# Performance work log

Measured on AMD Instinct MI355X. Metric: run time of the kernel, lower is better.

## Reference

```python
import jax, jax.numpy as jnp
import numpy as np

WIDTH = 2048
NUM_HEADS = 16
HEAD_DIM = WIDTH // NUM_HEADS
WINDOW = 1024
B, T = 4, 2048
MIN_LOGIT = -2.3819763e+38
MAX_WAVELENGTH = 10000.0


def apply_rope(x, positions):
    # x: [b, t, n, h]; RoPE on first half of h, pass-through second half
    b, t, n, h = x.shape
    x_rope, x_pass = jnp.split(x, 2, axis=-1)
    half = x_rope.shape[-1] // 2
    freq_exponents = 2.0 * jnp.arange(half, dtype=jnp.float32) / (2 * half)
    inv_freq = MAX_WAVELENGTH ** (-freq_exponents)  # [half]
    sinusoid = positions.astype(jnp.float32).reshape(1, t, 1, 1) * inv_freq  # [1,t,1,half]
    sin = jnp.sin(sinusoid).astype(x.dtype)
    cos = jnp.cos(sinusoid).astype(x.dtype)
    x1, x2 = jnp.split(x_rope, 2, axis=-1)
    return jnp.concatenate([x1 * cos - x2 * sin, x2 * cos + x1 * sin, x_pass], axis=-1)


def setup_inputs() -> dict:
    key = jax.random.key(0)
    ks = jax.random.split(key, 6)
    x = jax.random.normal(ks[0], (B, T, WIDTH), dtype=jnp.float32)
    segment_pos = jnp.arange(T, dtype=jnp.int32)
    # forward-pass mask: single segment, causal + window
    pos = jnp.arange(T)
    attention_mask = (pos[:, None] >= pos[None, :]) & (pos[:, None] <= pos[None, :] + WINDOW)
    std = np.sqrt(1.0 / WIDTH)
    wq = jax.random.normal(ks[1], (WIDTH, WIDTH), dtype=jnp.float32) * std
    wk = jax.random.normal(ks[2], (HEAD_DIM, WIDTH), dtype=jnp.float32) * std
    wv = jax.random.normal(ks[3], (HEAD_DIM, WIDTH), dtype=jnp.float32) * std
    w_out = jax.random.normal(ks[4], (WIDTH, WIDTH), dtype=jnp.float32) * std
    b_out = jnp.zeros((WIDTH,), dtype=jnp.float32)
    return {"x": x, "segment_pos": segment_pos, "attention_mask": attention_mask,
            "wq": wq, "wk": wk, "wv": wv, "w_out": w_out, "b_out": b_out}


def reference(x, segment_pos, attention_mask, wq, wk, wv, w_out, b_out):
    b, t, _ = x.shape
    q = (x @ wq.T).reshape(b, t, NUM_HEADS, HEAD_DIM)  # [b,t,n,h]
    k = (x @ wk.T).reshape(b, t, 1, HEAD_DIM)          # single shared KV head (MQA)
    v = x @ wv.T                                        # [b,t,h]
    q = apply_rope(q, segment_pos)
    k = apply_rope(k, segment_pos)[:, :, 0]             # [b,t,h]
    logits = jnp.einsum('btnh,bsh->bnts', q, k).astype(jnp.float32) * (HEAD_DIM ** -0.5)
    logits = jnp.where(attention_mask[None, None], logits, MIN_LOGIT)
    probs = jax.nn.softmax(logits, axis=-1).astype(x.dtype)
    encoded = jnp.einsum('bnts,bsh->btnh', probs, v).reshape(b, t, WIDTH)
    return encoded @ w_out.T + b_out
```

## Files before the change

### kernel.cpp

```cpp
#include <hip/hip_runtime.h>
#include <stdint.h>


#define WIDTH_ 2048
#define NHEADS_ 16
#define HD_ 128
#define WINDOW_ 1024
#define B_ 4
#define T_ 2048
#define MROWS_ (B_ * T_)
#define NQKV_ (WIDTH_ + 2 * HD_)

typedef float f32x4 __attribute__((ext_vector_type(4)));
typedef __bf16 bf16x8 __attribute__((ext_vector_type(8)));
typedef float f32x4v __attribute__((ext_vector_type(4)));
typedef unsigned short u16;
typedef unsigned int u32;

__device__ __forceinline__ u16 f2bf(float x) {
  u32 u = __builtin_bit_cast(u32, x);
  return (u16)((u + 0x7FFFu + ((u >> 16) & 1u)) >> 16);
}
__device__ __forceinline__ float bf2f(u16 b) {
  u32 u = ((u32)b) << 16;
  return __builtin_bit_cast(float, u);
}
__device__ __forceinline__ u32 pack2bf(float a, float b) {
  union { __bf16 h[2]; u32 u; } c;
  c.h[0] = (__bf16)a; c.h[1] = (__bf16)b;
  return c.u;
}

__device__ __forceinline__ f32x4 mfma16(bf16x8 a, bf16x8 b, f32x4 c) {
  return __builtin_amdgcn_mfma_f32_16x16x32_bf16(a, b, c, 0, 0, 0);
}

#define GLL16(gp, lp)                                          \
  __builtin_amdgcn_global_load_lds(                            \
      (const __attribute__((address_space(1))) void*)(gp),     \
      (__attribute__((address_space(3))) void*)(lp), 16, 0, 0)

#define CSC_ 0.12753101296631838f

__global__ __launch_bounds__(256) void cvt_f32_bf16(const float* __restrict__ src,
                                                    u16* __restrict__ dst, int n4) {
  int i = blockIdx.x * blockDim.x + threadIdx.x;
  int stride = gridDim.x * blockDim.x;
  for (; i < n4; i += stride) {
    f32x4v v = *reinterpret_cast<const f32x4v*>(src + 4 * (size_t)i);
    u32 lo = (u32)f2bf(v[0]) | ((u32)f2bf(v[1]) << 16);
    u32 hi = (u32)f2bf(v[2]) | ((u32)f2bf(v[3]) << 16);
    uint2 o;
    o.x = lo; o.y = hi;
    *reinterpret_cast<uint2*>(dst + 4 * (size_t)i) = o;
  }
}

__global__ __launch_bounds__(256) void cvt_weights(const float* __restrict__ wq,
                                                   const float* __restrict__ wk,
                                                   const float* __restrict__ wv,
                                                   const float* __restrict__ wo,
                                                   u16* __restrict__ wqkv,
                                                   u16* __restrict__ wob) {
  const int NQ = WIDTH_ * WIDTH_ / 4;
  const int NK = HD_ * WIDTH_ / 4;
  const int total = 2 * NQ + 2 * NK;
  int i = blockIdx.x * blockDim.x + threadIdx.x;
  int stride = gridDim.x * blockDim.x;
  for (; i < total; i += stride) {
    const float* s;
    u16* d;
    int j;
    if (i < NQ) { s = wq; d = wqkv; j = i; }
    else if (i < NQ + NK) { s = wk; d = wqkv + (size_t)WIDTH_ * WIDTH_; j = i - NQ; }
    else if (i < NQ + 2 * NK) { s = wv; d = wqkv + (size_t)(WIDTH_ + HD_) * WIDTH_; j = i - NQ - NK; }
    else { s = wo; d = wob; j = i - NQ - 2 * NK; }
    f32x4v v = *reinterpret_cast<const f32x4v*>(s + 4 * (size_t)j);
    uint2 o;
    o.x = (u32)f2bf(v[0]) | ((u32)f2bf(v[1]) << 16);
    o.y = (u32)f2bf(v[2]) | ((u32)f2bf(v[3]) << 16);
    *reinterpret_cast<uint2*>(d + 4 * (size_t)j) = o;
  }
}

template <bool F32OUT>
__global__ __launch_bounds__(256) void gemm_bt(const u16* __restrict__ A,
                                               const u16* __restrict__ W,
                                               void* __restrict__ Cout,
                                               const float* __restrict__ bias,
                                               int M, int N, int K) {
  __shared__ alignas(16) u16 As[128 * 32];
  __shared__ alignas(16) u16 Bs[128 * 32];
  const int tid = threadIdx.x;
  const int wid = tid >> 6, lane = tid & 63;
  const int g = lane >> 4, lr = lane & 15;
  const int m0 = blockIdx.y << 7, n0 = blockIdx.x << 7;
  const int wm = wid >> 1, wn = wid & 1;

  const f32x4 vzero = {0.f, 0.f, 0.f, 0.f};
  f32x4 acc[4][4];
#pragma unroll
  for (int i = 0; i < 4; i++)
#pragma unroll
    for (int j = 0; j < 4; j++) acc[i][j] = vzero;

  const int c0 = wid * 2, c1 = wid * 2 + 1;
  const int lrow = lane >> 2;
  const int lcol = (lane & 3) * 8;
  const u16* a0 = A + (size_t)(m0 + c0 * 16 + lrow) * K + lcol;
  const u16* a1 = A + (size_t)(m0 + c1 * 16 + lrow) * K + lcol;
  const u16* b0 = W + (size_t)(n0 + c0 * 16 + lrow) * K + lcol;
  const u16* b1 = W + (size_t)(n0 + c1 * 16 + lrow) * K + lcol;

  for (int k0 = 0; k0 < K; k0 += 32) {
    __syncthreads();
    GLL16(a0 + k0, &As[c0 * 512]);
    GLL16(a1 + k0, &As[c1 * 512]);
    GLL16(b0 + k0, &Bs[c0 * 512]);
    GLL16(b1 + k0, &Bs[c1 * 512]);
    __syncthreads();

    bf16x8 af[4], bfv[4];
#pragma unroll
    for (int mi = 0; mi < 4; mi++)
      af[mi] = *(const bf16x8*)&As[(wm * 64 + mi * 16 + lr) * 32 + g * 8];
#pragma unroll
    for (int ni = 0; ni < 4; ni++)
      bfv[ni] = *(const bf16x8*)&Bs[(wn * 64 + ni * 16 + lr) * 32 + g * 8];
#pragma unroll
    for (int mi = 0; mi < 4; mi++)
#pragma unroll
      for (int ni = 0; ni < 4; ni++)
        acc[mi][ni] = mfma16(af[mi], bfv[ni], acc[mi][ni]);
  }

#pragma unroll
  for (int mi = 0; mi < 4; mi++) {
    int row = m0 + wm * 64 + mi * 16 + g * 4;
#pragma unroll
    for (int ni = 0; ni < 4; ni++) {
      int col = n0 + wn * 64 + ni * 16 + lr;
#pragma unroll
      for (int r = 0; r < 4; r++) {
        float v = acc[mi][ni][r];
        if (F32OUT) {
          ((float*)Cout)[(size_t)(row + r) * N + col] = v + bias[col];
        } else {
          ((u16*)Cout)[(size_t)(row + r) * N + col] = f2bf(v);
        }
      }
    }
  }
}

template <bool F32OUT>
__global__ __launch_bounds__(512, 2) void gemm256(const u16* __restrict__ A,
                                                  const u16* __restrict__ W,
                                                  void* __restrict__ Cout,
                                                  const float* __restrict__ bias,
                                                  int M, int N, int K) {
  __shared__ alignas(16) u16 As[3][256 * 32];
  __shared__ alignas(16) u16 Bs[3][256 * 32];
  const int tid = threadIdx.x;
  const int wid = tid >> 6, lane = tid & 63;
  const int g = lane >> 4, lr = lane & 15;
  const int wm = wid >> 2, wn = wid & 3;

  const int nwg = gridDim.x;
  const int o = blockIdx.x;
  const int wg = (o & 7) * (nwg >> 3) + (o >> 3);
  const int NT = N >> 8;
  const int mt = wg / NT, nt = wg % NT;
  const int m0 = mt << 8, n0 = nt << 8;

  const u16* pa[2];
  const u16* pb[2];
#pragma unroll
  for (int j = 0; j < 2; j++) {
    int row = wid * 32 + j * 16 + (lane >> 2);
    int sc = (lane & 3) ^ ((row >> 1) & 3);
    pa[j] = A + (size_t)(m0 + row) * K + sc * 8;
    pb[j] = W + (size_t)(n0 + row) * K + sc * 8;
  }
  const int ldsoff = wid * 2048;

  const f32x4 vzero = {0.f, 0.f, 0.f, 0.f};
  f32x4 acc[8][4];
#pragma unroll
  for (int i = 0; i < 8; i++)
#pragma unroll
    for (int j = 0; j < 4; j++) acc[i][j] = vzero;

#define STAGE_A(bi, k0)                                        \
  do {                                                         \
    GLL16(pa[0] + (k0), (char*)As[bi] + ldsoff);               \
    GLL16(pa[1] + (k0), (char*)As[bi] + ldsoff + 1024);        \
  } while (0)
#define STAGE_B(bi, k0)                                        \
  do {                                                         \
    GLL16(pb[0] + (k0), (char*)Bs[bi] + ldsoff);               \
    GLL16(pb[1] + (k0), (char*)Bs[bi] + ldsoff + 1024);        \
  } while (0)

  STAGE_A(0, 0); STAGE_B(0, 0);
  STAGE_A(1, 32); STAGE_B(1, 32);
  asm volatile("s_waitcnt vmcnt(4)" ::: "memory");
  __builtin_amdgcn_sched_barrier(0);
  __builtin_amdgcn_s_barrier();

  const int ntk = K >> 5;
  int cur = 0;
  for (int t = 0; t < ntk; ++t) {
    const int nx2 = (cur + 2 >= 3) ? cur - 1 : cur + 2;
    const char* aB = (const char*)As[cur];
    const char* bB = (const char*)Bs[cur];
    const bool pre = (t + 2 < ntk);

    bf16x8 bfv[4], af[4];
#pragma unroll
    for (int ni = 0; ni < 4; ni++) {
      int row = wn * 64 + ni * 16 + lr;
      bfv[ni] = *(const bf16x8*)(bB + row * 64 + ((g ^ ((row >> 1) & 3)) << 4));
    }
#pragma unroll
    for (int mi = 0; mi < 4; mi++) {
      int row = wm * 128 + mi * 16 + lr;
      af[mi] = *(const bf16x8*)(aB + row * 64 + ((g ^ ((row >> 1) & 3)) << 4));
    }
    if (pre) STAGE_A(nx2, (t + 2) << 5);
    __builtin_amdgcn_s_barrier();
    asm volatile("s_waitcnt lgkmcnt(0)" ::: "memory");
    __builtin_amdgcn_sched_barrier(0);
    __builtin_amdgcn_s_setprio(1);
#pragma unroll
    for (int mi = 0; mi < 4; mi++)
#pragma unroll
      for (int ni = 0; ni < 4; ni++)
        acc[mi][ni] = mfma16(af[mi], bfv[ni], acc[mi][ni]);
    __builtin_amdgcn_s_setprio(0);
    __builtin_amdgcn_s_barrier();

    bf16x8 af2[4];
#pragma unroll
    for (int mi = 0; mi < 4; mi++) {
      int row = wm * 128 + 64 + mi * 16 + lr;
      af2[mi] = *(const bf16x8*)(aB + row * 64 + ((g ^ ((row >> 1) & 3)) << 4));
    }
    if (pre) STAGE_B(nx2, (t + 2) << 5);
    __builtin_amdgcn_s_barrier();
    asm volatile("s_waitcnt lgkmcnt(0)" ::: "memory");
    __builtin_amdgcn_sched_barrier(0);
    __builtin_amdgcn_s_setprio(1);
#pragma unroll
    for (int mi = 0; mi < 4; mi++)
#pragma unroll
      for (int ni = 0; ni < 4; ni++)
        acc[mi + 4][ni] = mfma16(af2[mi], bfv[ni], acc[mi + 4][ni]);
    __builtin_amdgcn_s_setprio(0);

    if (pre) {
      asm volatile("s_waitcnt vmcnt(4)" ::: "memory");
    } else if (t + 1 < ntk) {
      asm volatile("s_waitcnt vmcnt(0)" ::: "memory");
    }
    __builtin_amdgcn_sched_barrier(0);
    __builtin_amdgcn_s_barrier();

    cur = (cur + 1 >= 3) ? 0 : cur + 1;
  }
#undef STAGE_A
#undef STAGE_B

#pragma unroll
  for (int mi = 0; mi < 8; mi++) {
    int row = m0 + wm * 128 + mi * 16 + g * 4;
#pragma unroll
    for (int ni = 0; ni < 4; ni++) {
      int col = n0 + wn * 64 + ni * 16 + lr;
#pragma unroll
      for (int r = 0; r < 4; r++) {
        float v = acc[mi][ni][r];
        if (F32OUT) {
          ((float*)Cout)[(size_t)(row + r) * N + col] = v + bias[col];
        } else {
          ((u16*)Cout)[(size_t)(row + r) * N + col] = f2bf(v);
        }
      }
    }
  }
}

__global__ __launch_bounds__(256) void rope_scatter(const u16* __restrict__ Qraw,
                                                    const u16* __restrict__ KVraw,
                                                    const int* __restrict__ segpos,
                                                    u16* __restrict__ Qb,
                                                    u16* __restrict__ Kb,
                                                    u16* __restrict__ VT) {
  const int row = blockIdx.x;
  const int b = row / T_, t = row % T_;
  const float pos = (float)segpos[t];
  const u16* qsrc = Qraw + (size_t)row * WIDTH_;
  const u16* kvsrc = KVraw + (size_t)row * 256;
  const int tid = threadIdx.x;
  const float L2_10K_OVER_32 = 0.4152410118609203f;

  for (int j = tid; j < NHEADS_ * 32; j += 256) {
    int h = j >> 5, d = j & 31;
    float inv = exp2f(-(float)d * L2_10K_OVER_32);
    float ang = pos * inv;
    float sn = sinf(ang), cs = cosf(ang);
    int c1 = h * HD_ + d, c2 = c1 + 32;
    float x1 = bf2f(qsrc[c1]), x2 = bf2f(qsrc[c2]);
    Qb[(size_t)row * WIDTH_ + c1] = f2bf((x1 * cs - x2 * sn) * CSC_);
    Qb[(size_t)row * WIDTH_ + c2] = f2bf((x2 * cs + x1 * sn) * CSC_);
  }
  for (int j = tid; j < NHEADS_ * 64; j += 256) {
    int h = j >> 6, d = j & 63;
    int c = h * HD_ + 64 + d;
    Qb[(size_t)row * WIDTH_ + c] = f2bf(bf2f(qsrc[c]) * CSC_);
  }
  if (tid < 32) {
    int d = tid;
    float inv = exp2f(-(float)d * L2_10K_OVER_32);
    float ang = pos * inv;
    float sn = sinf(ang), cs = cosf(ang);
    float x1 = bf2f(kvsrc[d]), x2 = bf2f(kvsrc[d + 32]);
    Kb[(size_t)row * HD_ + d] = f2bf(x1 * cs - x2 * sn);
    Kb[(size_t)row * HD_ + d + 32] = f2bf(x2 * cs + x1 * sn);
  } else if (tid >= 64 && tid < 128) {
    int d = tid;
    Kb[(size_t)row * HD_ + d] = kvsrc[d];
  }
  for (int j = tid; j < HD_; j += 256) {
    VT[((size_t)b * HD_ + j) * T_ + t] = kvsrc[HD_ + j];
  }
}

__global__ __launch_bounds__(512, 4) void attn(const u16* __restrict__ Qb,
                                               const u16* __restrict__ Kb,
                                               const u16* __restrict__ VT,
                                               u16* __restrict__ Eb) {
  __shared__ alignas(16) u16 Ks[2][64 * 128];
  __shared__ alignas(16) u16 Vs[2][128 * 64];
  __shared__ alignas(16) u16 Ps[8][16 * 64];

  const int tid = threadIdx.x;
  const int wid = tid >> 6, lane = tid & 63;
  const int g = lane >> 4, lr = lane & 15;

  const int bid = blockIdx.x;
  const int grp = bid >> 4;
  const int b = grp >> 4, n = grp & 15;
  const int qt = ((bid & 15) + b * 4) & 15;
  const int q0b = qt * 128;
  const int q0w = q0b + wid * 16;

  const char* kptr = (const char*)(Kb + (size_t)b * T_ * HD_);
  const char* vptr = (const char*)(VT + (size_t)b * HD_ * T_);

  const char* srcb[4];
  int smul, dst0;
  if (wid < 4) {
    smul = HD_ * 2;
#pragma unroll
    for (int i = 0; i < 4; i++) {
      int row = wid * 16 + i * 4 + (lane >> 4);
      int c = (lane & 15) << 4;
      srcb[i] = kptr + (size_t)row * 256 + (c ^ ((row & 7) << 4));
    }
    dst0 = wid * 4096;
  } else {
    smul = 2;
#pragma unroll
    for (int i = 0; i < 4; i++) {
      int row = (wid - 4) * 32 + i * 8 + (lane >> 3);
      int c = (lane & 7) << 4;
      srcb[i] = vptr + (size_t)row * (T_ * 2) + (c ^ ((row & 7) << 4));
    }
    dst0 = (wid - 4) * 4096;
  }

  bf16x8 qf[4];
  {
    const u16* qrow = Qb + (size_t)(b * T_ + q0w + lr) * WIDTH_ + n * HD_;
#pragma unroll
    for (int kk = 0; kk < 4; kk++) qf[kk] = *(const bf16x8*)(qrow + kk * 32 + g * 8);
  }

  const f32x4 vzero = {0.f, 0.f, 0.f, 0.f};
  f32x4 eacc[8];
#pragma unroll
  for (int i = 0; i < 8; i++) eacc[i] = vzero;
  float m_r = -1e30f, l_r = 0.f;

  const int sbeg = (q0b > WINDOW_) ? (q0b - WINDOW_) : 0;
  const int nt = (q0b + 127 - sbeg) / 64 + 1;

  char* Pw = (char*)Ps[wid];
  const int swz = (lr & 7) << 4;
  const int q = q0w + lr;

  auto STAGE = [&](int s0, int buf) {
    char* dbase = (wid < 4) ? ((char*)Ks[buf] + dst0) : ((char*)Vs[buf] + dst0);
#pragma unroll
    for (int i = 0; i < 4; i++) {
      GLL16(srcb[i] + (size_t)s0 * smul, dbase + i * 1024);
    }
  };

  STAGE(sbeg, 0);
  __syncthreads();

  for (int t = 0; t < nt; ++t) {
    const int s0 = sbeg + t * 64;
    const int cur = t & 1;
    if (t + 1 < nt) STAGE(s0 + 64, cur ^ 1);

    const bool active = (s0 <= q0w + 15) && (s0 + 63 >= q0w - WINDOW_);
    if (active) {
      const char* kB = (const char*)Ks[cur];
      const char* vB = (const char*)Vs[cur];
      f32x4 sacc[4];
#pragma unroll
      for (int h = 0; h < 4; h++) sacc[h] = vzero;
#pragma unroll
      for (int h = 0; h < 4; h++) {
        const int krow = h * 16 + lr;
#pragma unroll
        for (int kk = 0; kk < 4; kk++) {
          bf16x8 kf = *(const bf16x8*)(kB + krow * 256 + ((kk * 64 + g * 16) ^ swz));
          sacc[h] = mfma16(kf, qf[kk], sacc[h]);
        }
      }

      const bool wint = (s0 + 63 <= q0w) && (s0 >= q0w + 15 - WINDOW_);
      float pm = -1e30f;
      if (wint) {
#pragma unroll
        for (int h = 0; h < 4; h++)
#pragma unroll
          for (int r = 0; r < 4; r++) pm = fmaxf(pm, sacc[h][r]);
      } else {
#pragma unroll
        for (int h = 0; h < 4; h++)
#pragma unroll
          for (int r = 0; r < 4; r++) {
            int s = s0 + h * 16 + g * 4 + r;
            bool ok = (s <= q) && (s + WINDOW_ >= q);
            float v = ok ? sacc[h][r] : -1e30f;
            sacc[h][r] = v;
            pm = fmaxf(pm, v);
          }
      }
      pm = fmaxf(pm, __shfl_xor(pm, 16));
      pm = fmaxf(pm, __shfl_xor(pm, 32));

      if (!__all(pm <= m_r + 8.f)) {
        float mnew = fmaxf(m_r, pm);
        float alpha = exp2f(m_r - mnew);
        m_r = mnew;
        l_r *= alpha;
        float aq[4];
#pragma unroll
        for (int r = 0; r < 4; r++) aq[r] = __shfl(alpha, g * 4 + r);
#pragma unroll
        for (int i = 0; i < 8; i++) {
          f32x4 e = eacc[i];
#pragma unroll
          for (int r = 0; r < 4; r++) e[r] *= aq[r];
          eacc[i] = e;
        }
      }
      float rs = 0.f;
#pragma unroll
      for (int h = 0; h < 4; h++)
#pragma unroll
        for (int r = 0; r < 4; r++) {
          float e = exp2f(sacc[h][r] - m_r);
          sacc[h][r] = e;
          rs += e;
        }
      rs += __shfl_xor(rs, 16);
      rs += __shfl_xor(rs, 32);
      l_r += rs;

#pragma unroll
      for (int h = 0; h < 4; h++) {
        int base = (lr * 128 + h * 32 + g * 8) ^ swz;
        uint2 w2;
        w2.x = pack2bf(sacc[h][0], sacc[h][1]);
        w2.y = pack2bf(sacc[h][2], sacc[h][3]);
        *(uint2*)(Pw + base) = w2;
      }
      bf16x8 pf0 = *(const bf16x8*)(Pw + ((lr * 128 + g * 16) ^ swz));
      bf16x8 pf1 = *(const bf16x8*)(Pw + ((lr * 128 + 64 + g * 16) ^ swz));

#pragma unroll
      for (int ht = 0; ht < 8; ht++) {
        const int vrow = ht * 16 + lr;
        bf16x8 vf0 = *(const bf16x8*)(vB + vrow * 128 + ((g * 16) ^ swz));
        bf16x8 vf1 = *(const bf16x8*)(vB + vrow * 128 + ((64 + g * 16) ^ swz));
        eacc[ht] = mfma16(pf0, vf0, eacc[ht]);
        eacc[ht] = mfma16(pf1, vf1, eacc[ht]);
      }
    }
    __syncthreads();
  }

  float lq[4];
#pragma unroll
  for (int r = 0; r < 4; r++) lq[r] = 1.f / __shfl(l_r, g * 4 + r);
#pragma unroll
  for (int ht = 0; ht < 8; ht++) {
#pragma unroll
    for (int r = 0; r < 4; r++) {
      int row = b * T_ + q0w + g * 4 + r;
      int col = n * HD_ + ht * 16 + lr;
      Eb[(size_t)row * WIDTH_ + col] = f2bf(eacc[ht][r] * lq[r]);
    }
  }
}

extern "C" void kernel_launch(void* const* d_in, const int* in_sizes, int n_in,
                              void* d_out, int out_size, void* d_ws, size_t ws_size,
                              hipStream_t stream) {
  (void)in_sizes; (void)n_in; (void)out_size; (void)ws_size;
  const float* x = (const float*)d_in[0];
  const int* segpos = (const int*)d_in[1];
  const float* wq = (const float*)d_in[3];
  const float* wk = (const float*)d_in[4];
  const float* wv = (const float*)d_in[5];
  const float* w_out = (const float*)d_in[6];
  const float* b_out = (const float*)d_in[7];

  char* p = (char*)d_ws;
  u16* xb = (u16*)p;    p += (size_t)MROWS_ * WIDTH_ * 2;
  u16* wqkv = (u16*)p;  p += (size_t)NQKV_ * WIDTH_ * 2;
  u16* wob = (u16*)p;   p += (size_t)WIDTH_ * WIDTH_ * 2;
  u16* qraw = (u16*)p;  p += (size_t)MROWS_ * WIDTH_ * 2;
  u16* kvraw = (u16*)p; p += (size_t)MROWS_ * 256 * 2;
  u16* qb = (u16*)p;    p += (size_t)MROWS_ * WIDTH_ * 2;
  u16* kb = (u16*)p;    p += (size_t)MROWS_ * HD_ * 2;
  u16* vt = (u16*)p;    p += (size_t)B_ * HD_ * T_ * 2;
  u16* eb = xb;

  cvt_f32_bf16<<<4096, 256, 0, stream>>>(x, xb, MROWS_ * WIDTH_ / 4);
  cvt_weights<<<2048, 256, 0, stream>>>(wq, wk, wv, w_out, wqkv, wob);

  gemm256<false><<<(MROWS_ / 256) * (WIDTH_ / 256), 512, 0, stream>>>(
      xb, wqkv, qraw, nullptr, MROWS_, WIDTH_, WIDTH_);
  gemm_bt<false><<<dim3(256 / 128, MROWS_ / 128), 256, 0, stream>>>(
      xb, wqkv + (size_t)WIDTH_ * WIDTH_, kvraw, nullptr, MROWS_, 256, WIDTH_);

  rope_scatter<<<MROWS_, 256, 0, stream>>>(qraw, kvraw, segpos, qb, kb, vt);
  attn<<<B_ * NHEADS_ * (T_ / 128), 512, 0, stream>>>(qb, kb, vt, eb);

  gemm256<true><<<(MROWS_ / 256) * (WIDTH_ / 256), 512, 0, stream>>>(
      eb, wob, d_out, b_out, MROWS_, WIDTH_, WIDTH_);
}
```

Baseline: 341.8 us.

## Fuse Q RoPE into attention and rework GEMM to 64-wide K pipeline

Q RoPE and scaling move out of the scatter kernel and into the attention kernel's Q-fragment load, so the separate Qb buffer is no longer written or re-read. The scatter kernel now handles only K and V with 128 threads. Separately, the 256x256 GEMM is restructured to stage 64-wide K slices in half-tiles, using double buffering and an 8-phase schedule in place of the triple-buffered 32-wide slices. The cost is redundant sin/cos evaluation per head in attention and a new, untested GEMM pipeline whose waitcnt accounting is intricate.

```diff
diff --git a/kernel.cpp b/kernel.cpp
--- a/kernel.cpp
+++ b/kernel.cpp
@@ -41,6 +41,7 @@
       (__attribute__((address_space(3))) void*)(lp), 16, 0, 0)
 
 #define CSC_ 0.12753101296631838f
+#define L2C_ 0.4152410118609203f
 
 __global__ __launch_bounds__(256) void cvt_f32_bf16(const float* __restrict__ src,
                                                     u16* __restrict__ dst, int n4) {
@@ -154,13 +155,13 @@
 }
 
 template <bool F32OUT>
-__global__ __launch_bounds__(512, 2) void gemm256(const u16* __restrict__ A,
-                                                  const u16* __restrict__ W,
-                                                  void* __restrict__ Cout,
-                                                  const float* __restrict__ bias,
-                                                  int M, int N, int K) {
-  __shared__ alignas(16) u16 As[3][256 * 32];
-  __shared__ alignas(16) u16 Bs[3][256 * 32];
+__global__ __launch_bounds__(512, 2) void gemm256p8(const u16* __restrict__ A,
+                                                    const u16* __restrict__ W,
+                                                    void* __restrict__ Cout,
+                                                    const float* __restrict__ bias,
+                                                    int M, int N, int K) {
+  __shared__ alignas(16) u16 As[2][2][128 * 64];
+  __shared__ alignas(16) u16 Bs[2][2][128 * 64];
   const int tid = threadIdx.x;
   const int wid = tid >> 6, lane = tid & 63;
   const int g = lane >> 4, lr = lane & 15;
@@ -177,12 +178,27 @@
   const u16* pb[2];
 #pragma unroll
   for (int j = 0; j < 2; j++) {
-    int row = wid * 32 + j * 16 + (lane >> 2);
-    int sc = (lane & 3) ^ ((row >> 1) & 3);
-    pa[j] = A + (size_t)(m0 + row) * K + sc * 8;
-    pb[j] = W + (size_t)(n0 + row) * K + sc * 8;
-  }
-  const int ldsoff = wid * 2048;
+    int ci = (wid + j * 8) * 64 + lane;
+    int ri = ci >> 3, c = ci & 7;
+    int colel = (c ^ (ri & 7)) * 8;
+    int rA = ((ri >> 6) << 7) + (ri & 63);
+    pa[j] = A + (size_t)(m0 + rA) * K + colel;
+    pb[j] = W + (size_t)(n0 + ri) * K + colel;
+  }
+  const int dstoff = wid * 1024;
+
+#define SA(bi, h, k0)                                                     \
+  do {                                                                    \
+    GLL16(pa[0] + (size_t)(h) * 64 * K + (k0), (char*)As[bi][h] + dstoff);\
+    GLL16(pa[1] + (size_t)(h) * 64 * K + (k0),                            \
+          (char*)As[bi][h] + dstoff + 8192);                              \
+  } while (0)
+#define SB(bi, h, k0)                                                     \
+  do {                                                                    \
+    GLL16(pb[0] + (size_t)(h) * 128 * K + (k0), (char*)Bs[bi][h] + dstoff);\
+    GLL16(pb[1] + (size_t)(h) * 128 * K + (k0),                           \
+          (char*)Bs[bi][h] + dstoff + 8192);                              \
+  } while (0)
 
   const f32x4 vzero = {0.f, 0.f, 0.f, 0.f};
   f32x4 acc[8][4];
@@ -191,85 +207,74 @@
 #pragma unroll
     for (int j = 0; j < 4; j++) acc[i][j] = vzero;
 
-#define STAGE_A(bi, k0)                                        \
-  do {                                                         \
-    GLL16(pa[0] + (k0), (char*)As[bi] + ldsoff);               \
-    GLL16(pa[1] + (k0), (char*)As[bi] + ldsoff + 1024);        \
-  } while (0)
-#define STAGE_B(bi, k0)                                        \
-  do {                                                         \
-    GLL16(pb[0] + (k0), (char*)Bs[bi] + ldsoff);               \
-    GLL16(pb[1] + (k0), (char*)Bs[bi] + ldsoff + 1024);        \
-  } while (0)
-
-  STAGE_A(0, 0); STAGE_B(0, 0);
-  STAGE_A(1, 32); STAGE_B(1, 32);
-  asm volatile("s_waitcnt vmcnt(4)" ::: "memory");
+  bf16x8 bfv[4][2];
+
+  auto LDA = [&](int bi, int mi, int kk) -> bf16x8 {
+    int h = mi >> 2;
+    int rb = wm * 64 + (mi & 3) * 16 + lr;
+    return *(const bf16x8*)((const char*)As[bi][h] + rb * 128 +
+                            (((kk * 4 + g) ^ (lr & 7)) << 4));
+  };
+  auto LDB = [&](int bi, int ni, int kk) -> bf16x8 {
+    int rb = (wn & 1) * 64 + ni * 16 + lr;
+    return *(const bf16x8*)((const char*)Bs[bi][wn >> 1] + rb * 128 +
+                            (((kk * 4 + g) ^ (lr & 7)) << 4));
+  };
+
+#define VM6 asm volatile("s_waitcnt vmcnt(6)" ::: "memory")
+#define VM0 asm volatile("s_waitcnt vmcnt(0)" ::: "memory")
+
+#define PHASE(bi, p, STAGES, VM)                                          \
+  {                                                                       \
+    if ((p) == 0) {                                                       \
+      for (int ni = 0; ni < 4; ni++)                                      \
+        for (int kk = 0; kk < 2; kk++) bfv[ni][kk] = LDB(bi, ni, kk);     \
+    }                                                                     \
+    bf16x8 a0k0 = LDA(bi, 2 * (p), 0);                                    \
+    bf16x8 a0k1 = LDA(bi, 2 * (p), 1);                                    \
+    bf16x8 a1k0 = LDA(bi, 2 * (p) + 1, 0);                                \
+    bf16x8 a1k1 = LDA(bi, 2 * (p) + 1, 1);                                \
+    STAGES;                                                               \
+    __builtin_amdgcn_s_barrier();                                         \
+    asm volatile("s_waitcnt lgkmcnt(0)" ::: "memory");                    \
+    __builtin_amdgcn_sched_barrier(0);                                    \
+    __builtin_amdgcn_s_setprio(1);                                        \
+    for (int ni = 0; ni < 4; ni++) {                                      \
+      acc[2 * (p)][ni] = mfma16(a0k0, bfv[ni][0], acc[2 * (p)][ni]);      \
+      acc[2 * (p)][ni] = mfma16(a0k1, bfv[ni][1], acc[2 * (p)][ni]);      \
+      acc[2 * (p) + 1][ni] = mfma16(a1k0, bfv[ni][0], acc[2 * (p) + 1][ni]); \
+      acc[2 * (p) + 1][ni] = mfma16(a1k1, bfv[ni][1], acc[2 * (p) + 1][ni]); \
+    }                                                                     \
+    __builtin_amdgcn_s_setprio(0);                                        \
+    VM;                                                                   \
+    __builtin_amdgcn_sched_barrier(0);                                    \
+    __builtin_amdgcn_s_barrier();                                         \
+  }
+
+  SA(0, 0, 0); SA(0, 1, 0); SB(0, 0, 0); SB(0, 1, 0);
+  SB(1, 0, 64); SB(1, 1, 64); SA(1, 0, 64);
+  VM6;
   __builtin_amdgcn_sched_barrier(0);
   __builtin_amdgcn_s_barrier();
 
-  const int ntk = K >> 5;
-  int cur = 0;
-  for (int t = 0; t < ntk; ++t) {
-    const int nx2 = (cur + 2 >= 3) ? cur - 1 : cur + 2;
-    const char* aB = (const char*)As[cur];
-    const char* bB = (const char*)Bs[cur];
-    const bool pre = (t + 2 < ntk);
-
-    bf16x8 bfv[4], af[4];
-#pragma unroll
-    for (int ni = 0; ni < 4; ni++) {
-      int row = wn * 64 + ni * 16 + lr;
-      bfv[ni] = *(const bf16x8*)(bB + row * 64 + ((g ^ ((row >> 1) & 3)) << 4));
-    }
-#pragma unroll
-    for (int mi = 0; mi < 4; mi++) {
-      int row = wm * 128 + mi * 16 + lr;
-      af[mi] = *(const bf16x8*)(aB + row * 64 + ((g ^ ((row >> 1) & 3)) << 4));
-    }
-    if (pre) STAGE_A(nx2, (t + 2) << 5);
-    __builtin_amdgcn_s_barrier();
-    asm volatile("s_waitcnt lgkmcnt(0)" ::: "memory");
-    __builtin_amdgcn_sched_barrier(0);
-    __builtin_amdgcn_s_setprio(1);
-#pragma unroll
-    for (int mi = 0; mi < 4; mi++)
-#pragma unroll
-      for (int ni = 0; ni < 4; ni++)
-        acc[mi][ni] = mfma16(af[mi], bfv[ni], acc[mi][ni]);
-    __builtin_amdgcn_s_setprio(0);
-    __builtin_amdgcn_s_barrier();
-
-    bf16x8 af2[4];
-#pragma unroll
-    for (int mi = 0; mi < 4; mi++) {
-      int row = wm * 128 + 64 + mi * 16 + lr;
-      af2[mi] = *(const bf16x8*)(aB + row * 64 + ((g ^ ((row >> 1) & 3)) << 4));
-    }
-    if (pre) STAGE_B(nx2, (t + 2) << 5);
-    __builtin_amdgcn_s_barrier();
-    asm volatile("s_waitcnt lgkmcnt(0)" ::: "memory");
-    __builtin_amdgcn_sched_barrier(0);
-    __builtin_amdgcn_s_setprio(1);
-#pragma unroll
-    for (int mi = 0; mi < 4; mi++)
-#pragma unroll
-      for (int ni = 0; ni < 4; ni++)
-        acc[mi + 4][ni] = mfma16(af2[mi], bfv[ni], acc[mi + 4][ni]);
-    __builtin_amdgcn_s_setprio(0);
-
-    if (pre) {
-      asm volatile("s_waitcnt vmcnt(4)" ::: "memory");
-    } else if (t + 1 < ntk) {
-      asm volatile("s_waitcnt vmcnt(0)" ::: "memory");
-    }
-    __builtin_amdgcn_sched_barrier(0);
-    __builtin_amdgcn_s_barrier();
-
-    cur = (cur + 1 >= 3) ? 0 : cur + 1;
-  }
-#undef STAGE_A
-#undef STAGE_B
+  const int half_iters = K >> 7;
+  for (int i = 0; i < half_iters; ++i) {
+    const bool pre = (i + 1 < half_iters);
+    const int kc = i << 7;
+    PHASE(0, 0, { SA(1, 1, kc + 64); }, );
+    PHASE(0, 1, { if (pre) SB(0, 0, kc + 128); }, );
+    PHASE(0, 2, { if (pre) SB(0, 1, kc + 128); }, );
+    PHASE(0, 3, { if (pre) SA(0, 0, kc + 128); }, if (pre) { VM6; } else { VM0; });
+    PHASE(1, 0, { if (pre) SA(0, 1, kc + 128); }, );
+    PHASE(1, 1, { if (pre) SB(1, 0, kc + 192); }, );
+    PHASE(1, 2, { if (pre) SB(1, 1, kc + 192); }, );
+    PHASE(1, 3, { if (pre) SA(1, 0, kc + 192); }, if (pre) { VM6; } else { VM0; });
+  }
+#undef PHASE
+#undef SA
+#undef SB
+#undef VM6
+#undef VM0
 
 #pragma unroll
   for (int mi = 0; mi < 8; mi++) {
@@ -290,38 +295,19 @@
   }
 }
 
-__global__ __launch_bounds__(256) void rope_scatter(const u16* __restrict__ Qraw,
-                                                    const u16* __restrict__ KVraw,
-                                                    const int* __restrict__ segpos,
-                                                    u16* __restrict__ Qb,
-                                                    u16* __restrict__ Kb,
-                                                    u16* __restrict__ VT) {
+__global__ __launch_bounds__(128) void kv_scatter(const u16* __restrict__ KVraw,
+                                                  const int* __restrict__ segpos,
+                                                  u16* __restrict__ Kb,
+                                                  u16* __restrict__ VT) {
   const int row = blockIdx.x;
   const int b = row / T_, t = row % T_;
   const float pos = (float)segpos[t];
-  const u16* qsrc = Qraw + (size_t)row * WIDTH_;
   const u16* kvsrc = KVraw + (size_t)row * 256;
   const int tid = threadIdx.x;
-  const float L2_10K_OVER_32 = 0.4152410118609203f;
-
-  for (int j = tid; j < NHEADS_ * 32; j += 256) {
-    int h = j >> 5, d = j & 31;
-    float inv = exp2f(-(float)d * L2_10K_OVER_32);
-    float ang = pos * inv;
-    float sn = sinf(ang), cs = cosf(ang);
-    int c1 = h * HD_ + d, c2 = c1 + 32;
-    float x1 = bf2f(qsrc[c1]), x2 = bf2f(qsrc[c2]);
-    Qb[(size_t)row * WIDTH_ + c1] = f2bf((x1 * cs - x2 * sn) * CSC_);
-    Qb[(size_t)row * WIDTH_ + c2] = f2bf((x2 * cs + x1 * sn) * CSC_);
-  }
-  for (int j = tid; j < NHEADS_ * 64; j += 256) {
-    int h = j >> 6, d = j & 63;
-    int c = h * HD_ + 64 + d;
-    Qb[(size_t)row * WIDTH_ + c] = f2bf(bf2f(qsrc[c]) * CSC_);
-  }
+
   if (tid < 32) {
     int d = tid;
-    float inv = exp2f(-(float)d * L2_10K_OVER_32);
+    float inv = exp2f(-(float)d * L2C_);
     float ang = pos * inv;
     float sn = sinf(ang), cs = cosf(ang);
     float x1 = bf2f(kvsrc[d]), x2 = bf2f(kvsrc[d + 32]);
@@ -331,12 +317,13 @@
     int d = tid;
     Kb[(size_t)row * HD_ + d] = kvsrc[d];
   }
-  for (int j = tid; j < HD_; j += 256) {
+  for (int j = tid; j < HD_; j += 128) {
     VT[((size_t)b * HD_ + j) * T_ + t] = kvsrc[HD_ + j];
   }
 }
 
-__global__ __launch_bounds__(512, 4) void attn(const u16* __restrict__ Qb,
+__global__ __launch_bounds__(512, 4) void attn(const u16* __restrict__ Qraw,
+                                               const int* __restrict__ segpos,
                                                const u16* __restrict__ Kb,
                                                const u16* __restrict__ VT,
                                                u16* __restrict__ Eb) {
@@ -354,6 +341,7 @@
   const int qt = ((bid & 15) + b * 4) & 15;
   const int q0b = qt * 128;
   const int q0w = q0b + wid * 16;
+  const int q = q0w + lr;
 
   const char* kptr = (const char*)(Kb + (size_t)b * T_ * HD_);
   const char* vptr = (const char*)(VT + (size_t)b * HD_ * T_);
@@ -382,9 +370,23 @@
 
   bf16x8 qf[4];
   {
-    const u16* qrow = Qb + (size_t)(b * T_ + q0w + lr) * WIDTH_ + n * HD_;
-#pragma unroll
-    for (int kk = 0; kk < 4; kk++) qf[kk] = *(const bf16x8*)(qrow + kk * 32 + g * 8);
+    const float pos = (float)segpos[q];
+    const u16* qp = Qraw + (size_t)(b * T_ + q) * WIDTH_ + n * HD_;
+    bf16x8 r0 = *(const bf16x8*)(qp + g * 8);
+    bf16x8 r1 = *(const bf16x8*)(qp + 32 + g * 8);
+    bf16x8 r2 = *(const bf16x8*)(qp + 64 + g * 8);
+    bf16x8 r3 = *(const bf16x8*)(qp + 96 + g * 8);
+#pragma unroll
+    for (int j = 0; j < 8; j++) {
+      float d = (float)(g * 8 + j);
+      float ang = pos * exp2f(-d * L2C_);
+      float sn = sinf(ang), cs = cosf(ang);
+      float x1 = (float)r0[j], x2 = (float)r1[j];
+      qf[0][j] = (__bf16)((x1 * cs - x2 * sn) * CSC_);
+      qf[1][j] = (__bf16)((x2 * cs + x1 * sn) * CSC_);
+      qf[2][j] = (__bf16)((float)r2[j] * CSC_);
+      qf[3][j] = (__bf16)((float)r3[j] * CSC_);
+    }
   }
 
   const f32x4 vzero = {0.f, 0.f, 0.f, 0.f};
@@ -398,7 +400,6 @@
 
   char* Pw = (char*)Ps[wid];
   const int swz = (lr & 7) << 4;
-  const int q = q0w + lr;
 
   auto STAGE = [&](int s0, int buf) {
     char* dbase = (wid < 4) ? ((char*)Ks[buf] + dst0) : ((char*)Vs[buf] + dst0);
@@ -539,7 +540,6 @@
   u16* wob = (u16*)p;   p += (size_t)WIDTH_ * WIDTH_ * 2;
   u16* qraw = (u16*)p;  p += (size_t)MROWS_ * WIDTH_ * 2;
   u16* kvraw = (u16*)p; p += (size_t)MROWS_ * 256 * 2;
-  u16* qb = (u16*)p;    p += (size_t)MROWS_ * WIDTH_ * 2;
   u16* kb = (u16*)p;    p += (size_t)MROWS_ * HD_ * 2;
   u16* vt = (u16*)p;    p += (size_t)B_ * HD_ * T_ * 2;
   u16* eb = xb;
@@ -547,14 +547,14 @@
   cvt_f32_bf16<<<4096, 256, 0, stream>>>(x, xb, MROWS_ * WIDTH_ / 4);
   cvt_weights<<<2048, 256, 0, stream>>>(wq, wk, wv, w_out, wqkv, wob);
 
-  gemm256<false><<<(MROWS_ / 256) * (WIDTH_ / 256), 512, 0, stream>>>(
+  gemm256p8<false><<<(MROWS_ / 256) * (WIDTH_ / 256), 512, 0, stream>>>(
       xb, wqkv, qraw, nullptr, MROWS_, WIDTH_, WIDTH_);
   gemm_bt<false><<<dim3(256 / 128, MROWS_ / 128), 256, 0, stream>>>(
       xb, wqkv + (size_t)WIDTH_ * WIDTH_, kvraw, nullptr, MROWS_, 256, WIDTH_);
 
-  rope_scatter<<<MROWS_, 256, 0, stream>>>(qraw, kvraw, segpos, qb, kb, vt);
-  attn<<<B_ * NHEADS_ * (T_ / 128), 512, 0, stream>>>(qb, kb, vt, eb);
-
-  gemm256<true><<<(MROWS_ / 256) * (WIDTH_ / 256), 512, 0, stream>>>(
+  kv_scatter<<<MROWS_, 128, 0, stream>>>(kvraw, segpos, kb, vt);
+  attn<<<B_ * NHEADS_ * (T_ / 128), 512, 0, stream>>>(qraw, segpos, kb, vt, eb);
+
+  gemm256p8<true><<<(MROWS_ / 256) * (WIDTH_ / 256), 512, 0, stream>>>(
       eb, wob, d_out, b_out, MROWS_, WIDTH_, WIDTH_);
 }
```

Measured after the change: 322.5 us. 1.06x faster.
